# Kernel optimization log

Measured on AMD Instinct MI355X. Metric: run time of the kernel, lower is better.

The kernel has to match this reference:

```python
import jax, jax.numpy as jnp
import numpy as np
import math

BS, T, C, H, W = 2, 3, 128, 48, 48
NH, NL, NPT, KS = 8, 3, 4, 3
DH = C // NH
LQ = T * H * W


def conv2d(x, w, b):
    y = jax.lax.conv_general_dilated(x, w, (1, 1), 'SAME', dimension_numbers=('NCHW', 'OIHW', 'NCHW'))
    return y + b[None, :, None, None]


def bilinear_sample(img, x, y, zeros_pad):
    # img: (B, C, H, W); x, y: (B, Q) pixel coords. zeros_pad -> grid_sample padding_mode='zeros', else 'border'.
    B, Cc, Hh, Ww = img.shape
    x0 = jnp.floor(x); y0 = jnp.floor(y)
    wx = x - x0; wy = y - y0
    flat = img.reshape(B, Cc, Hh * Ww)
    def corner(xi, yi, wgt):
        if zeros_pad:
            wgt = wgt * ((xi >= 0) & (xi <= Ww - 1) & (yi >= 0) & (yi <= Hh - 1)).astype(img.dtype)
        xc = jnp.clip(xi, 0, Ww - 1).astype(jnp.int32)
        yc = jnp.clip(yi, 0, Hh - 1).astype(jnp.int32)
        g = jnp.take_along_axis(flat, (yc * Ww + xc)[:, None, :], axis=2)  # (B, C, Q)
        return g * wgt[:, None, :]
    return (corner(x0, y0, (1 - wx) * (1 - wy)) + corner(x0 + 1, y0, wx * (1 - wy))
            + corner(x0, y0 + 1, (1 - wx) * wy) + corner(x0 + 1, y0 + 1, wx * wy))


def warp_w_mask(x, flo):
    # grid_sample(border, align_corners=True): normalized coords round-trip to raw pixel coords grid+flow
    B, Cc, Hh, Ww = x.shape
    vx = (jnp.arange(Ww, dtype=x.dtype)[None, None, :] + flo[:, 0]).reshape(B, -1)
    vy = (jnp.arange(Hh, dtype=x.dtype)[None, :, None] + flo[:, 1]).reshape(B, -1)
    out = bilinear_sample(x, vx, vy, False).reshape(B, Cc, Hh, Ww)
    m = bilinear_sample(jnp.ones((B, 1, Hh, Ww), x.dtype), vx, vy, True).reshape(B, 1, Hh, Ww)
    m = jnp.where(m < 0.999, 0.0, 1.0).astype(x.dtype)
    return out * m


def flow_guid_offset(ff, fb, off):
    N = off.shape[0]
    off = off.reshape(N, NL, H * W, NH, NL, NPT, 2)
    ff01, ff12 = ff[:, 0], ff[:, 1]
    ff02 = ff01 + warp_w_mask(ff12, ff01)
    fb10, fb21 = fb[:, 0], fb[:, 1]
    fb20 = fb21 + warp_w_mask(fb10, fb21)
    seq = lambda f: f.transpose(0, 2, 3, 1).reshape(N, H * W, 2)
    z = jnp.zeros((N, H * W, 2), off.dtype)
    adds = jnp.stack([
        jnp.stack([z, seq(ff01), seq(ff02)], axis=2),
        jnp.stack([seq(fb10), z, seq(ff12)], axis=2),
        jnp.stack([seq(fb20), seq(fb21), z], axis=2)], axis=1)  # (N, 3, HW, 3, 2)
    off = off + adds[:, :, :, None, :, None, :]
    return off.reshape(N, LQ, NH, NL, NPT, 2)


def reference(query, input_flatten, reference_points, flow_forward, flow_backward,
              w_off, b_off, w_attn, b_attn, w_val, b_val, w_out, b_out,
              input_spatial_shapes, input_level_start_index, input_padding_mask):
    bs, t, c, h, w = query.shape
    N = bs
    value = conv2d(input_flatten.reshape(bs * t, c, h, w), w_val, b_val)
    off = conv2d(query.reshape(bs * t, c, h, w), w_off, b_off)
    attn = conv2d(query.reshape(bs * t, c, h, w), w_attn, b_attn)
    tohw = lambda x: x.reshape(bs, t, -1, h * w).transpose(0, 1, 3, 2).reshape(bs, t * h * w, -1)
    value, off, attn = tohw(value), tohw(off), tohw(attn)
    value = jnp.where(input_padding_mask[..., None], 0.0, value)
    value = value.reshape(N, t * h * w, NH, DH)
    off = off.reshape(N, LQ, NH, NL, NPT, 2)
    off = flow_guid_offset(flow_forward, flow_backward, off)
    attn = jax.nn.softmax(attn.reshape(N, LQ, NH, NL * NPT), axis=-1).reshape(N, LQ, NH, NL, NPT)
    normalizer = jnp.stack([input_spatial_shapes[:, 1], input_spatial_shapes[:, 0]], -1).astype(query.dtype)
    loc = reference_points[:, :, None, :, None, :] + off / normalizer[None, None, None, :, None, :]
    # multi-level deformable sampling: grid_sample(bilinear, zeros padding, align_corners=False)
    vb = value.reshape(N, NL, h * w, NH, DH).transpose(0, 1, 3, 4, 2).reshape(N * NL * NH, DH, h, w)
    px = (loc[..., 0] * w - 0.5).transpose(0, 3, 2, 1, 4).reshape(N * NL * NH, LQ * NPT)
    py = (loc[..., 1] * h - 0.5).transpose(0, 3, 2, 1, 4).reshape(N * NL * NH, LQ * NPT)
    samp = bilinear_sample(vb, px, py, True).reshape(N, NL, NH, DH, LQ, NPT)
    out = jnp.einsum('nlhdqp,nqhlp->nqhd', samp, attn).reshape(N, LQ, c)
    out = out.reshape(bs, t, h, w, c).transpose(0, 1, 4, 2, 3).reshape(bs * t, c, h, w)
    out = conv2d(out, w_out, b_out).reshape(bs, t, c, h, w)
    return out


def setup_inputs():
    key = jax.random.key(0)
    ks = jax.random.split(key, 9)
    query = jax.random.normal(ks[0], (BS, T, C, H, W), jnp.float32)
    input_flatten = jax.random.normal(ks[1], (BS, T, C, H, W), jnp.float32)
    reference_points = jax.random.uniform(ks[2], (BS, LQ, NL, 2), jnp.float32)
    flow_forward = jax.random.normal(ks[3], (BS, 2, 2, H, W), jnp.float32) * 2.0
    flow_backward = jax.random.normal(ks[4], (BS, 2, 2, H, W), jnp.float32) * 2.0
    co = NH * NL * NPT * 2
    w_off = jax.random.normal(ks[5], (co, C, KS, KS), jnp.float32) * 0.01
    thetas = np.arange(NH, dtype=np.float32) * (2.0 * math.pi / NH)
    g = np.stack([np.cos(thetas), np.sin(thetas)], -1)
    g = g / np.abs(g).max(-1, keepdims=True)
    g = np.tile(g.reshape(NH, 1, 1, 2), (1, NL, NPT, 1)) * (np.arange(NPT, dtype=np.float32) + 1.0).reshape(1, 1, NPT, 1)
    b_off = jnp.asarray(g.reshape(-1))
    ca = NH * NL * NPT
    w_attn = jax.random.normal(ks[6], (ca, C, KS, KS), jnp.float32) * 0.01
    b_attn = jnp.zeros((ca,), jnp.float32)
    s = 1.0 / np.sqrt(C * KS * KS)
    w_val = jax.random.normal(ks[7], (C, C, KS, KS), jnp.float32) * s
    b_val = jnp.zeros((C,), jnp.float32)
    w_out = jax.random.normal(ks[8], (C, C, KS, KS), jnp.float32) * s
    b_out = jnp.zeros((C,), jnp.float32)
    input_spatial_shapes = jnp.array([[H, W]] * NL, jnp.int32)
    input_level_start_index = jnp.array([0, H * W, 2 * H * W], jnp.int32)
    input_padding_mask = jnp.zeros((BS, LQ), bool)
    return {'query': query, 'input_flatten': input_flatten, 'reference_points': reference_points,
            'flow_forward': flow_forward, 'flow_backward': flow_backward,
            'w_off': w_off, 'b_off': b_off, 'w_attn': w_attn, 'b_attn': b_attn,
            'w_val': w_val, 'b_val': b_val, 'w_out': w_out, 'b_out': b_out,
            'input_spatial_shapes': input_spatial_shapes,
            'input_level_start_index': input_level_start_index,
            'input_padding_mask': input_padding_mask}
```

## Files before the change

kernel.cpp:

```cpp
#include <hip/hip_runtime.h>
#include <math.h>

#define WID 48
#define HW 2304
#define PAD 50

typedef _Float16 half8 __attribute__((ext_vector_type(8)));
typedef _Float16 half2 __attribute__((ext_vector_type(2)));
typedef float f32x4 __attribute__((ext_vector_type(4)));

__device__ __forceinline__ void gload_lds16(const void* g, void* l) {
  __builtin_amdgcn_global_load_lds((const __attribute__((address_space(1))) void*)g,
                                   (__attribute__((address_space(3))) void*)l, 16, 0, 0);
}

__global__ __launch_bounds__(256) void prep_kernel(
    const float* __restrict__ q, const float* __restrict__ f,
    _Float16* __restrict__ xq, _Float16* __restrict__ xf,
    const float* __restrict__ wv, const float* __restrict__ wo,
    const float* __restrict__ wa, const float* __restrict__ wu,
    _Float16* __restrict__ wt,
    const float* __restrict__ ff, const float* __restrict__ fb,
    float* __restrict__ adds,
    _Float16* __restrict__ wsh) {
  __shared__ _Float16 plds[48 * 136];
  const int b = blockIdx.x;
  const int tid = threadIdx.x;

  if (b < 576) {
    const int buf = b / 288;
    const int rem = b - buf * 288;
    const int img = rem / 48, y = rem - img * 48;
    const float* src = buf ? f : q;
    _Float16* dst = buf ? xf : xq;

    const int c = tid >> 1;
    const int seg = tid & 1;
    const float* rowp = src + ((size_t)img * 128 + c) * HW + y * WID + seg * 24;
    f32x4 v[6];
#pragma unroll
    for (int k = 0; k < 6; ++k) v[k] = *(const f32x4*)(rowp + 4 * k);
#pragma unroll
    for (int k = 0; k < 6; ++k)
#pragma unroll
      for (int e = 0; e < 4; ++e)
        plds[(seg * 24 + 4 * k + e) * 136 + c] = (_Float16)v[k][e];
    __syncthreads();

    _Float16* dstp = dst + (((size_t)img * PAD + y + 1) * PAD + 1) * 128;
#pragma unroll
    for (int k = 0; k < 3; ++k) {
      int m = tid + 256 * k;
      int px = m >> 4, c0 = (m & 15) << 3;
      half8 h = *(const half8*)(plds + px * 136 + c0);
      *(half8*)(dstp + (size_t)m * 8) = h;
    }

  } else if (b < 3024) {
    int gi = (b - 576) * 256 + tid;
    if (gi >= 544 * 1152) return;
    int row = gi / 1152, k = gi - row * 1152;
    int tap = k >> 7, ci = k & 127;
    const float* src; int co;
    if (row < 128)      { src = wv; co = row; }
    else if (row < 320) { src = wo; co = row - 128; }
    else if (row < 416) { src = wa; co = row - 320; }
    else                { src = wu; co = row - 416; }
    wt[gi] = (_Float16)src[((size_t)co * 128 + ci) * 9 + tap];

  } else if (b < 3325) {
    int gi = (b - 3024) * 256 + tid;
    const int IMG_ELE = PAD * PAD * 128;
    half8 z = {};
    if (gi < 75264) {
      int bi = gi / 3136;
      int r = gi - bi * 3136;
      int p = r >> 4;
      int cc = (r & 15) << 3;
      int y, x;
      if (p < 50)       { y = 0;           x = p; }
      else if (p < 100) { y = 49;          x = p - 50; }
      else if (p < 148) { y = p - 100 + 1; x = 0; }
      else              { y = p - 148 + 1; x = 49; }
      *(half8*)(wsh + (size_t)bi * IMG_ELE + ((size_t)y * PAD + x) * 128 + cc) = z;
    } else if (gi < 76864) {
      int r = gi - 75264;
      *(half8*)(wsh + (size_t)24 * IMG_ELE + (size_t)r * 8) = z;
    }

  } else {
    int idx = (b - 3325) * 256 + tid;
    if (idx >= 2 * HW) return;
    int n = idx / HW, hw = idx - n * HW;
    int y = hw / WID, x = hw - y * WID;

    const float* F = ff + (size_t)n * 4 * HW;
    const float* B = fb + (size_t)n * 4 * HW;

    float ff01x = F[hw],          ff01y = F[HW + hw];
    float ff12x = F[2 * HW + hw], ff12y = F[3 * HW + hw];
    float fb10x = B[hw],          fb10y = B[HW + hw];
    float fb21x = B[2 * HW + hw], fb21y = B[3 * HW + hw];

    auto warp2 = [&](const float* cx, const float* cy, float flox, float floy,
                     float& ox, float& oy) {
      float sx = (float)x + flox, sy = (float)y + floy;
      float fx = floorf(sx), fy = floorf(sy);
      int x0 = (int)fx, y0 = (int)fy;
      float wx = sx - fx, wy = sy - fy;
      float w00 = (1.f - wx) * (1.f - wy), w10 = wx * (1.f - wy);
      float w01 = (1.f - wx) * wy,         w11 = wx * wy;
      auto inside = [](int xi, int yi) {
        return (xi >= 0 && xi <= WID - 1 && yi >= 0 && yi <= WID - 1) ? 1.f : 0.f;
      };
      float m = w00 * inside(x0, y0)     + w10 * inside(x0 + 1, y0) +
                w01 * inside(x0, y0 + 1) + w11 * inside(x0 + 1, y0 + 1);
      float mm = (m < 0.999f) ? 0.f : 1.f;
      auto cl = [](int v) { return v < 0 ? 0 : (v > WID - 1 ? WID - 1 : v); };
      int xa = cl(x0), xb = cl(x0 + 1), ya = cl(y0), yb = cl(y0 + 1);
      int i00 = ya * WID + xa, i10 = ya * WID + xb;
      int i01 = yb * WID + xa, i11 = yb * WID + xb;
      ox = mm * (w00 * cx[i00] + w10 * cx[i10] + w01 * cx[i01] + w11 * cx[i11]);
      oy = mm * (w00 * cy[i00] + w10 * cy[i10] + w01 * cy[i01] + w11 * cy[i11]);
    };

    float wfx, wfy;
    warp2(F + 2 * HW, F + 3 * HW, ff01x, ff01y, wfx, wfy);
    float ff02x = ff01x + wfx, ff02y = ff01y + wfy;
    float wbx, wby;
    warp2(B, B + HW, fb21x, fb21y, wbx, wby);
    float fb20x = fb21x + wbx, fb20y = fb21y + wby;

    auto W_ = [&](int t, int l, float vx, float vy) {
      size_t o = (((size_t)(n * 3 + t) * 3 + l) * HW + hw) * 2;
      adds[o] = vx; adds[o + 1] = vy;
    };
    W_(0, 0, 0.f, 0.f);     W_(0, 1, ff01x, ff01y); W_(0, 2, ff02x, ff02y);
    W_(1, 0, fb10x, fb10y); W_(1, 1, 0.f, 0.f);     W_(1, 2, ff12x, ff12y);
    W_(2, 0, fb20x, fb20y); W_(2, 1, fb21x, fb21y); W_(2, 2, 0.f, 0.f);
  }
}

#define CONV_BUF_ELE (96 * 64 + 64 * 64)

__device__ __forceinline__ void conv_body(
    int bx, const _Float16* __restrict__ xpad, const _Float16* __restrict__ wt,
    const float* __restrict__ bias0, const float* __restrict__ bias1, int bsplit,
    int CO, int co0, int layout, void* __restrict__ outp, _Float16* lds) {
  const int tid = threadIdx.x;
  const int w = tid >> 6, lane = tid & 63;
  const int img = bx / 24, rp = bx - img * 24;
  const int y0 = rp * 2;

  const int pxh = w & 1, coh = w >> 1;

  f32x4 acc[3][2] = {};

  const int lr8 = lane >> 3;
  const int lc  = lane & 7;

  auto stage = [&](int s, _Float16* l) {
    const int tap = s >> 1, ci0 = (s & 1) << 6;
    const int dy = tap / 3, dx = tap - dy * 3;
    _Float16* lA = l;
    _Float16* lB = l + 96 * 64;
#pragma unroll
    for (int it = 0; it < 3; ++it) {
      int i = w * 3 + it;
      int r = 8 * i + lr8;
      int cs = lc ^ (r & 7);
      int up = (r >= 48) ? 1 : 0;
      int yy = y0 + up + dy;
      int xx = (r - 48 * up) + dx;
      const _Float16* src = xpad + (((size_t)(img * PAD + yy)) * PAD + xx) * 128 + ci0 + cs * 8;
      gload_lds16(src, lA + i * 512);
    }
#pragma unroll
    for (int jt = 0; jt < 2; ++jt) {
      int j = w * 2 + jt;
      int r = 8 * j + lr8;
      int cs = lc ^ (r & 7);
      int co = co0 + r; if (co >= CO) co = CO - 1;
      const _Float16* src = wt + (size_t)co * 1152 + tap * 128 + ci0 + cs * 8;
      gload_lds16(src, lB + j * 512);
    }
  };

  _Float16* cur = lds;
  _Float16* nxt = lds + CONV_BUF_ELE;

  stage(0, cur);
  __syncthreads();

  const int lrow = lane & 15, lk = lane >> 4;
#pragma unroll
  for (int s = 0; s < 18; ++s) {
    if (s < 17) stage(s + 1, nxt);

    _Float16* lA = cur;
    _Float16* lB = cur + 96 * 64;
    __builtin_amdgcn_s_setprio(1);
#pragma unroll
    for (int sub = 0; sub < 2; ++sub) {
      int kc = sub * 4 + lk;
      half8 a[3], bb[2];
#pragma unroll
      for (int m = 0; m < 3; ++m) {
        int r = 48 * pxh + 16 * m + lrow;
        a[m] = *(const half8*)(lA + r * 64 + ((kc ^ (r & 7)) * 8));
      }
#pragma unroll
      for (int n = 0; n < 2; ++n) {
        int r = 32 * coh + 16 * n + lrow;
        bb[n] = *(const half8*)(lB + r * 64 + ((kc ^ (r & 7)) * 8));
      }
#pragma unroll
      for (int m = 0; m < 3; ++m)
#pragma unroll
        for (int n = 0; n < 2; ++n)
          acc[m][n] = __builtin_amdgcn_mfma_f32_16x16x32_f16(a[m], bb[n], acc[m][n], 0, 0, 0);
    }
    __builtin_amdgcn_s_setprio(0);

    __syncthreads();
    _Float16* t = cur; cur = nxt; nxt = t;
  }

  const int lg = lane >> 4;
#pragma unroll
  for (int m = 0; m < 3; ++m) {
#pragma unroll
    for (int n = 0; n < 2; ++n) {
      int co = co0 + 32 * coh + 16 * n + lrow;
      if (co >= CO) continue;
      float bv = (co < bsplit) ? bias0[co] : bias1[co - bsplit];
#pragma unroll
      for (int r = 0; r < 4; ++r) {
        int pl = 48 * pxh + 16 * m + 4 * lg + r;
        int pix = rp * 96 + pl;
        float v = acc[m][n][r] + bv;
        if (layout == 1) {
          ((_Float16*)outp)[((size_t)img * HW + pix) * CO + co] = (_Float16)v;
        } else if (layout == 2) {
          int yy = pix / WID, xx = pix - yy * WID;
          ((_Float16*)outp)[(((size_t)img * PAD + yy + 1) * PAD + xx + 1) * 128 + co] = (_Float16)v;
        } else {
          ((float*)outp)[((size_t)img * CO + co) * HW + pix] = v;
        }
      }
    }
  }
}

__global__ __launch_bounds__(256) void conv_offattn_value(
    const _Float16* __restrict__ xq, const _Float16* __restrict__ xf,
    const _Float16* __restrict__ wt,
    const float* __restrict__ b_off, const float* __restrict__ b_attn,
    const float* __restrict__ b_val,
    _Float16* __restrict__ offattn, _Float16* __restrict__ vpad) {
  __shared__ _Float16 lds[2 * CONV_BUF_ELE];
  const int y = blockIdx.y;
  if (y < 5) {
    conv_body(blockIdx.x, xq, wt + (size_t)128 * 1152, b_off, b_attn, 192,
              288, y * 64, 1, offattn, lds);
  } else {
    conv_body(blockIdx.x, xf, wt, b_val, b_val, 128,
              128, (y - 5) * 64, 2, vpad, lds);
  }
}

__global__ __launch_bounds__(256) void conv_out(
    const _Float16* __restrict__ xout, const _Float16* __restrict__ wt,
    const float* __restrict__ b_out, float* __restrict__ out) {
  __shared__ _Float16 lds[2 * CONV_BUF_ELE];
  conv_body(blockIdx.x, xout, wt, b_out, b_out, 128, 128, blockIdx.y * 64, 0,
            out, lds);
}

__global__ __launch_bounds__(256) void sample_kernel(
    const _Float16* __restrict__ vpad,
    const _Float16* __restrict__ offattn,
    const float* __restrict__ refpts, const float* __restrict__ adds,
    _Float16* __restrict__ xout) {
  __shared__ float Wlds[16][13][4];
  __shared__ int   IBlds[16][12];
  const int tid = threadIdx.x;
  const int pixg = blockIdx.x * 2 + (tid >> 7);
  const int g = tid >> 4;
  const int h = g & 7;
  const int d = tid & 15;
  const int img = pixg / HW, hw = pixg - img * HW;
  const int n = img / 3, t = img - n * 3;

  const _Float16* rec = offattn + ((size_t)img * HW + hw) * 288;

  const int i = (d < 12) ? d : 11;
  const int l = i >> 2;

  half2 o2 = *(const half2*)(rec + (h * 12 + i) * 2);
  float lgt = (float)rec[192 + h * 12 + i];
  if (d >= 12) lgt = -1e30f;

  const float* addp = adds + (((size_t)(n * 3 + t) * 3 + l) * HW + hw) * 2;
  const float* rp = refpts + ((size_t)(n * 3 + t) * HW + hw) * 6 + l * 2;

  float px = fmaf(rp[0], 48.f, -0.5f) + (float)o2[0] + addp[0];
  float py = fmaf(rp[1], 48.f, -0.5f) + (float)o2[1] + addp[1];
  px = fminf(fmaxf(px, -1.f), 48.f);
  py = fminf(fmaxf(py, -1.f), 48.f);
  float fx = floorf(px), fy = floorf(py);
  int x0 = (int)fx, y0 = (int)fy;
  float wx = px - fx, wy = py - fy;
  float w00 = (1.f - wx) * (1.f - wy), w10 = wx * (1.f - wy);
  float w01 = (1.f - wx) * wy,         w11 = wx * wy;

  float mx = lgt;
#pragma unroll
  for (int m = 8; m >= 1; m >>= 1) mx = fmaxf(mx, __shfl_xor(mx, m, 16));
  float e = __expf(lgt - mx);
  float s = e;
#pragma unroll
  for (int m = 8; m >= 1; m >>= 1) s += __shfl_xor(s, m, 16);
  float aw = e * __builtin_amdgcn_rcpf(s);
  w00 *= aw; w10 *= aw; w01 *= aw; w11 *= aw;

  int ib = (((n * 3 + l) * PAD + (y0 + 1)) * PAD + (x0 + 1)) * 128 + h * 16;

  if (d < 12) {
    f32x4 w4 = {w00, w10, w01, w11};
    *(f32x4*)&Wlds[g][d][0] = w4;
    IBlds[g][d] = ib;
  }
  __syncthreads();

  float acc = 0.f;
#pragma unroll
  for (int j = 0; j < 12; ++j) {
    f32x4 W = *(const f32x4*)&Wlds[g][j][0];
    int jb = IBlds[g][j];
    const _Float16* vp = vpad + jb + d;
    acc = fmaf(W[0], (float)vp[0], acc);
    acc = fmaf(W[1], (float)vp[128], acc);
    acc = fmaf(W[2], (float)vp[PAD * 128], acc);
    acc = fmaf(W[3], (float)vp[PAD * 128 + 128], acc);
  }

  int y = hw / WID, x = hw - y * WID;
  xout[(((size_t)img * PAD + y + 1) * PAD + x + 1) * 128 + h * 16 + d] = (_Float16)acc;
}

extern "C" void kernel_launch(void* const* d_in, const int* in_sizes, int n_in,
                              void* d_out, int out_size, void* d_ws, size_t ws_size,
                              hipStream_t stream) {
  const float* query         = (const float*)d_in[0];
  const float* input_flatten = (const float*)d_in[1];
  const float* refpts        = (const float*)d_in[2];
  const float* ff            = (const float*)d_in[3];
  const float* fb            = (const float*)d_in[4];
  const float* w_off         = (const float*)d_in[5];
  const float* b_off         = (const float*)d_in[6];
  const float* w_attn        = (const float*)d_in[7];
  const float* b_attn        = (const float*)d_in[8];
  const float* w_val         = (const float*)d_in[9];
  const float* b_val         = (const float*)d_in[10];
  const float* w_out         = (const float*)d_in[11];
  const float* b_out         = (const float*)d_in[12];
  float* out = (float*)d_out;

  char* ws = (char*)d_ws;
  const size_t PADSZ = (size_t)6 * PAD * PAD * 128 * sizeof(_Float16);
  const size_t GUARD = (size_t)2 * PAD * 128 * sizeof(_Float16);
  _Float16* xq      = (_Float16*)(ws);
  _Float16* xf      = (_Float16*)(ws + PADSZ);
  _Float16* xout    = (_Float16*)(ws + 2 * PADSZ);
  _Float16* vpad    = (_Float16*)(ws + 3 * PADSZ);
  _Float16* wt      = (_Float16*)(ws + 4 * PADSZ + GUARD);
  _Float16* offattn = (_Float16*)(ws + 4 * PADSZ + GUARD + 1253376);
  float*    adds    = (float*)   (ws + 4 * PADSZ + GUARD + 1253376 + 7962624);

  prep_kernel<<<3343, 256, 0, stream>>>(query, input_flatten, xq, xf,
                                        w_val, w_off, w_attn, w_out, wt,
                                        ff, fb, adds, (_Float16*)ws);

  conv_offattn_value<<<dim3(144, 7), 256, 0, stream>>>(xq, xf, wt,
                                                       b_off, b_attn, b_val,
                                                       offattn, vpad);

  sample_kernel<<<6912, 256, 0, stream>>>(vpad, offattn, refpts, adds, xout);

  conv_out<<<dim3(144, 2), 256, 0, stream>>>(xout, wt + (size_t)416 * 1152,
                                             b_out, out);
}
```

Before: 66.96 us.

## Load full padded input halo once into LDS and reuse across all conv taps

The implicit-GEMM conv used to reload a shifted 96x64 input tile from global memory for each of the 18 tap/channel stages. It now loads the whole 4-row by 50-column by 128-channel padded halo into LDS once, with an XOR swizzle, and indexes it per tap with dy/dx offsets. Only the weight tiles are still double-buffered per stage. This cuts redundant global-to-LDS traffic about ninefold, but the up-front load is not overlapped with compute, and LDS use grows to about 69 KB, which may lower occupancy.

```diff
diff --git a/kernel.cpp b/kernel.cpp
--- a/kernel.cpp
+++ b/kernel.cpp
@@ -141,7 +141,9 @@
   }
 }
 
-#define CONV_BUF_ELE (96 * 64 + 64 * 64)
+#define LDSA_CHUNKS 3328
+#define LDSA_HALF  (LDSA_CHUNKS * 8)
+#define LDSB_HALF  4096
 
 __device__ __forceinline__ void conv_body(
     int bx, const _Float16* __restrict__ xpad, const _Float16* __restrict__ wt,
@@ -159,46 +161,46 @@
   const int lr8 = lane >> 3;
   const int lc  = lane & 7;
 
-  auto stage = [&](int s, _Float16* l) {
+  _Float16* lA  = lds;
+  _Float16* lB0 = lds + LDSA_HALF;
+  _Float16* lB1 = lds + LDSA_HALF + LDSB_HALF;
+
+  const _Float16* span = xpad + ((size_t)(img * PAD + y0)) * PAD * 128;
+#pragma unroll
+  for (int it = 0; it < 13; ++it) {
+    int i = w * 13 + it;
+    int o = i * 64 + lane;
+    int p = o >> 4, c = o & 15;
+    gload_lds16(span + p * 128 + ((c ^ (p & 7)) << 3), lA + i * 512);
+  }
+
+  auto stageB = [&](int s, _Float16* lB) {
     const int tap = s >> 1, ci0 = (s & 1) << 6;
-    const int dy = tap / 3, dx = tap - dy * 3;
-    _Float16* lA = l;
-    _Float16* lB = l + 96 * 64;
-#pragma unroll
-    for (int it = 0; it < 3; ++it) {
-      int i = w * 3 + it;
-      int r = 8 * i + lr8;
-      int cs = lc ^ (r & 7);
-      int up = (r >= 48) ? 1 : 0;
-      int yy = y0 + up + dy;
-      int xx = (r - 48 * up) + dx;
-      const _Float16* src = xpad + (((size_t)(img * PAD + yy)) * PAD + xx) * 128 + ci0 + cs * 8;
-      gload_lds16(src, lA + i * 512);
-    }
 #pragma unroll
     for (int jt = 0; jt < 2; ++jt) {
       int j = w * 2 + jt;
       int r = 8 * j + lr8;
       int cs = lc ^ (r & 7);
       int co = co0 + r; if (co >= CO) co = CO - 1;
-      const _Float16* src = wt + (size_t)co * 1152 + tap * 128 + ci0 + cs * 8;
-      gload_lds16(src, lB + j * 512);
+      gload_lds16(wt + (size_t)co * 1152 + tap * 128 + ci0 + cs * 8, lB + j * 512);
     }
   };
 
-  _Float16* cur = lds;
-  _Float16* nxt = lds + CONV_BUF_ELE;
-
-  stage(0, cur);
+  stageB(0, lB0);
   __syncthreads();
 
   const int lrow = lane & 15, lk = lane >> 4;
+  const int pbase = pxh * 50 + lrow;
 #pragma unroll
   for (int s = 0; s < 18; ++s) {
-    if (s < 17) stage(s + 1, nxt);
-
-    _Float16* lA = cur;
-    _Float16* lB = cur + 96 * 64;
+    _Float16* bcur = (s & 1) ? lB1 : lB0;
+    _Float16* bnxt = (s & 1) ? lB0 : lB1;
+    if (s < 17) stageB(s + 1, bnxt);
+
+    const int tap = s >> 1;
+    const int dy = tap / 3, dx = tap - dy * 3;
+    const int choff = (s & 1) << 3;
+
     __builtin_amdgcn_s_setprio(1);
 #pragma unroll
     for (int sub = 0; sub < 2; ++sub) {
@@ -206,13 +208,14 @@
       half8 a[3], bb[2];
 #pragma unroll
       for (int m = 0; m < 3; ++m) {
-        int r = 48 * pxh + 16 * m + lrow;
-        a[m] = *(const half8*)(lA + r * 64 + ((kc ^ (r & 7)) * 8));
+        int p = pbase + 16 * m + dy * 50 + dx;
+        int qc = (choff + kc) ^ (p & 7);
+        a[m] = *(const half8*)(lA + p * 128 + qc * 8);
       }
 #pragma unroll
       for (int n = 0; n < 2; ++n) {
         int r = 32 * coh + 16 * n + lrow;
-        bb[n] = *(const half8*)(lB + r * 64 + ((kc ^ (r & 7)) * 8));
+        bb[n] = *(const half8*)(bcur + r * 64 + ((kc ^ (r & 7)) * 8));
       }
 #pragma unroll
       for (int m = 0; m < 3; ++m)
@@ -223,7 +226,6 @@
     __builtin_amdgcn_s_setprio(0);
 
     __syncthreads();
-    _Float16* t = cur; cur = nxt; nxt = t;
   }
 
   const int lg = lane >> 4;
@@ -252,13 +254,15 @@
   }
 }
 
+#define CONV_LDS_TOT (LDSA_HALF + 2 * LDSB_HALF)
+
 __global__ __launch_bounds__(256) void conv_offattn_value(
     const _Float16* __restrict__ xq, const _Float16* __restrict__ xf,
     const _Float16* __restrict__ wt,
     const float* __restrict__ b_off, const float* __restrict__ b_attn,
     const float* __restrict__ b_val,
     _Float16* __restrict__ offattn, _Float16* __restrict__ vpad) {
-  __shared__ _Float16 lds[2 * CONV_BUF_ELE];
+  __shared__ _Float16 lds[CONV_LDS_TOT];
   const int y = blockIdx.y;
   if (y < 5) {
     conv_body(blockIdx.x, xq, wt + (size_t)128 * 1152, b_off, b_attn, 192,
@@ -272,7 +276,7 @@
 __global__ __launch_bounds__(256) void conv_out(
     const _Float16* __restrict__ xout, const _Float16* __restrict__ wt,
     const float* __restrict__ b_out, float* __restrict__ out) {
-  __shared__ _Float16 lds[2 * CONV_BUF_ELE];
+  __shared__ _Float16 lds[CONV_LDS_TOT];
   conv_body(blockIdx.x, xout, wt, b_out, b_out, 128, 128, blockIdx.y * 64, 0,
             out, lds);
 }
```

Result: slower. 68.49 us (+2.3%).
